# Performance work log

Measured on AMD Instinct MI355X. Metric: run time of the kernel, lower is better.

The kernel has to match this reference:

```python
import jax, jax.numpy as jnp
import numpy as np

EPS = 1e-5

def conv1x1(x, w, b):
    # x: [B,C,H,W], w: [O,C], b: [O]
    return jnp.einsum('bchw,oc->bohw', x, w) + b[None, :, None, None]

def bn(x, g, b, m, v):
    # eval-mode BatchNorm2d over channel axis 1
    s = g / jnp.sqrt(v + EPS)
    return (x - m[None, :, None, None]) * s[None, :, None, None] + b[None, :, None, None]

def setup_inputs() -> dict:
    key = jax.random.key(0)
    ks = jax.random.split(key, 12)
    B, C, Ci, H, W = 8, 512, 256, 64, 64
    d = {}
    d['x'] = jax.random.normal(ks[0], (B, C, H, W), jnp.float32)
    d['theta_w'] = jax.random.normal(ks[1], (Ci, C), jnp.float32) * (C ** -0.5)
    d['theta_b'] = jnp.zeros((Ci,), jnp.float32)
    d['theta_bn_g'] = jax.random.uniform(ks[2], (Ci,), jnp.float32, 0.5, 1.5)
    d['theta_bn_b'] = jax.random.normal(ks[3], (Ci,), jnp.float32) * 0.1
    d['theta_bn_m'] = jnp.zeros((Ci,), jnp.float32)
    d['theta_bn_v'] = jnp.ones((Ci,), jnp.float32)
    d['phi_w'] = jax.random.normal(ks[4], (Ci, C), jnp.float32) * (C ** -0.5)
    d['phi_b'] = jnp.zeros((Ci,), jnp.float32)
    d['phi_bn_g'] = jax.random.uniform(ks[5], (Ci,), jnp.float32, 0.5, 1.5)
    d['phi_bn_b'] = jax.random.normal(ks[6], (Ci,), jnp.float32) * 0.1
    d['phi_bn_m'] = jnp.zeros((Ci,), jnp.float32)
    d['phi_bn_v'] = jnp.ones((Ci,), jnp.float32)
    d['g_w'] = jax.random.normal(ks[7], (Ci, C), jnp.float32) * (C ** -0.5)
    d['g_b'] = jnp.zeros((Ci,), jnp.float32)
    d['wz_w'] = jax.random.normal(ks[8], (C, Ci), jnp.float32) * (Ci ** -0.5)
    d['wz_b'] = jnp.zeros((C,), jnp.float32)
    d['wz_bn_g'] = jax.random.uniform(ks[9], (C,), jnp.float32, 0.5, 1.5)
    d['wz_bn_b'] = jax.random.normal(ks[10], (C,), jnp.float32) * 0.1
    d['wz_bn_m'] = jnp.zeros((C,), jnp.float32)
    d['wz_bn_v'] = jnp.ones((C,), jnp.float32)
    return d

def reference(x, theta_w, theta_b, theta_bn_g, theta_bn_b, theta_bn_m, theta_bn_v,
              phi_w, phi_b, phi_bn_g, phi_bn_b, phi_bn_m, phi_bn_v,
              g_w, g_b, wz_w, wz_b, wz_bn_g, wz_bn_b, wz_bn_m, wz_bn_v):
    B, C, H, W = x.shape
    Ci = theta_w.shape[0]
    N = H * W
    scale = Ci ** -0.5
    th = bn(conv1x1(x, theta_w, theta_b), theta_bn_g, theta_bn_b, theta_bn_m, theta_bn_v).reshape(B, Ci, N)
    ph = bn(conv1x1(x, phi_w, phi_b), phi_bn_g, phi_bn_b, phi_bn_m, phi_bn_v).reshape(B, Ci, N)
    gx = conv1x1(x, g_w, g_b).reshape(B, Ci, N)
    # attn[b,n,m] = <theta[:,n], phi[:,m]> * scale, softmax over m (fp32 as in source)
    attn = jax.nn.softmax(jnp.einsum('bcn,bcm->bnm', th, ph) * scale, axis=-1)
    y = jnp.einsum('bnm,bcm->bcn', attn, gx).reshape(B, Ci, H, W)
    out = bn(conv1x1(y, wz_w, wz_b), wz_bn_g, wz_bn_b, wz_bn_m, wz_bn_v) + x
    return out
```

## Files before the change

kernel.cpp:

```cpp
#include <hip/hip_runtime.h>
#include <hip/hip_bf16.h>

typedef __attribute__((ext_vector_type(8))) short bf16x8;
typedef __attribute__((ext_vector_type(4))) float f32x4;
typedef __attribute__((ext_vector_type(16))) float f32x16;
typedef __attribute__((ext_vector_type(4))) unsigned short us4;
typedef __attribute__((ext_vector_type(8))) unsigned short us8;
typedef __attribute__((ext_vector_type(4))) unsigned int u32x4;

#define B_  8
#define C_  512
#define CI_ 256
#define N_  4096

__device__ __forceinline__ unsigned short f2b(float f) {
  unsigned u = __float_as_uint(f);
  u += 0x7FFFu + ((u >> 16) & 1u);
  return (unsigned short)(u >> 16);
}

__device__ __forceinline__ unsigned pkbf16(float lo, float hi) {
  union { __hip_bfloat162 h2; unsigned u; } cv;
  cv.h2 = __float22bfloat162_rn(make_float2(lo, hi));
  return cv.u;
}

__device__ __forceinline__ f32x4 mfma16(bf16x8 a, bf16x8 b, f32x4 c) {
  return __builtin_amdgcn_mfma_f32_16x16x32_bf16(a, b, c, 0, 0, 0);
}
__device__ __forceinline__ f32x16 mfma32(bf16x8 a, bf16x8 b, f32x16 c) {
  return __builtin_amdgcn_mfma_f32_32x32x16_bf16(a, b, c, 0, 0, 0);
}

__device__ __forceinline__ void gld16(const void* g, void* l) {
  __builtin_amdgcn_global_load_lds(
      (const __attribute__((address_space(1))) unsigned int*)g,
      (__attribute__((address_space(3))) unsigned int*)l, 16, 0, 0);
}

__global__ void fold_kernel(
  const float* __restrict__ thw, const float* __restrict__ thb,
  const float* __restrict__ thg, const float* __restrict__ thbb,
  const float* __restrict__ thm, const float* __restrict__ thv,
  const float* __restrict__ phw, const float* __restrict__ phb,
  const float* __restrict__ phg, const float* __restrict__ phbb,
  const float* __restrict__ phm, const float* __restrict__ phv,
  const float* __restrict__ gw,  const float* __restrict__ gb,
  const float* __restrict__ wzw, const float* __restrict__ wzb,
  const float* __restrict__ wzg, const float* __restrict__ wzbb,
  const float* __restrict__ wzm, const float* __restrict__ wzv,
  unsigned short* __restrict__ thW, unsigned short* __restrict__ phW,
  unsigned short* __restrict__ gW,  unsigned short* __restrict__ wzW,
  float* __restrict__ bTh, float* __restrict__ bPh,
  float* __restrict__ bG,  float* __restrict__ bWz)
{
  int i = blockIdx.x * 256 + threadIdx.x;
  const int WSZ = CI_ * C_;
  if (i < WSZ) { int o = i >> 9; thW[i] = f2b(thw[i] * (thg[o] * rsqrtf(thv[o] + 1e-5f))); return; }
  i -= WSZ;
  if (i < WSZ) { int o = i >> 9; phW[i] = f2b(phw[i] * (phg[o] * rsqrtf(phv[o] + 1e-5f))); return; }
  i -= WSZ;
  if (i < WSZ) { gW[i] = f2b(gw[i]); return; }
  i -= WSZ;
  if (i < WSZ) { int o = i >> 8; wzW[i] = f2b(wzw[i] * (wzg[o] * rsqrtf(wzv[o] + 1e-5f))); return; }
  i -= WSZ;
  if (i < CI_) { float s = thg[i] * rsqrtf(thv[i] + 1e-5f); bTh[i] = (thb[i] - thm[i]) * s + thbb[i]; return; }
  i -= CI_;
  if (i < CI_) { float s = phg[i] * rsqrtf(phv[i] + 1e-5f); bPh[i] = (phb[i] - phm[i]) * s + phbb[i]; return; }
  i -= CI_;
  if (i < CI_) { bG[i] = gb[i]; return; }
  i -= CI_;
  if (i < C_)  { float s = wzg[i] * rsqrtf(wzv[i] + 1e-5f); bWz[i] = (wzb[i] - wzm[i]) * s + wzbb[i]; return; }
}

__global__ __launch_bounds__(256) void transpose_cast(
  const float* __restrict__ x, unsigned short* __restrict__ xT)
{
  __shared__ float tl[64][68];
  const int b = blockIdx.z, c0 = blockIdx.y * 64, n0 = blockIdx.x * 64;
  const int t = threadIdx.x;
  const int r = t >> 2, q = (t & 3) * 16;
  const float* src = x + ((size_t)(b * C_ + c0 + r)) * N_ + n0 + q;
#pragma unroll
  for (int i = 0; i < 4; i++)
    *(f32x4*)&tl[r][q + i * 4] = *(const f32x4*)(src + i * 4);
  __syncthreads();
  unsigned short* dst = xT + ((size_t)(b * N_ + n0 + r)) * C_ + c0 + q;
  us8 o0, o1;
#pragma unroll
  for (int i = 0; i < 8; i++) o0[i] = f2b(tl[q + i][r]);
#pragma unroll
  for (int i = 0; i < 8; i++) o1[i] = f2b(tl[q + 8 + i][r]);
  *(us8*)dst = o0;
  *(us8*)(dst + 8) = o1;
}

template <int MODE>
__global__ __launch_bounds__(256, 2) void gemm_bt(
  const unsigned short* __restrict__ A,
  const unsigned short* __restrict__ Bm,
  const float* __restrict__ bias,
  const float* __restrict__ resid,
  void* __restrict__ outp,
  int Mdim, int Ndim, int Kdim)
{
  __shared__ __align__(16) unsigned short Al[2][128][64];
  __shared__ __align__(16) unsigned short Bl[2][128][64];
  const int b = blockIdx.z;
  const int m0 = blockIdx.y * 128;
  const int n0 = blockIdx.x * 128;
  const int t = threadIdx.x;
  const int w = t >> 6, l = t & 63, l15 = l & 15, g = l >> 4;
  const int wm = w >> 1, wn = w & 1;
  const int eg = l15 & 7;
  const unsigned short* Bb = Bm + (size_t)b * Ndim * Kdim;
  f32x4 acc[4][4];
#pragma unroll
  for (int i = 0; i < 4; i++)
#pragma unroll
    for (int j = 0; j < 4; j++) acc[i][j] = (f32x4){0.f, 0.f, 0.f, 0.f};

  int aoff[4], boff[4];
#pragma unroll
  for (int i = 0; i < 4; i++) {
    int j = w * 4 + i;
    int row = j * 8 + (l >> 3);
    int sw = ((l & 7) ^ (l >> 3)) * 8;
    aoff[i] = (m0 + row) * Kdim + sw;
    boff[i] = (n0 + row) * Kdim + sw;
  }

#define GSTAGE(bufv, k0v) do { \
    _Pragma("unroll") \
    for (int i_ = 0; i_ < 4; i_++) { \
      gld16(A  + aoff[i_] + (k0v), (unsigned char*)&Al[bufv][0][0] + (w * 4 + i_) * 1024); \
      gld16(Bb + boff[i_] + (k0v), (unsigned char*)&Bl[bufv][0][0] + (w * 4 + i_) * 1024); \
    } \
  } while (0)

  const int nk = Kdim >> 6;
  GSTAGE(0, 0);
  __syncthreads();
  for (int kk = 0; kk < nk; kk++) {
    if (kk + 1 < nk) GSTAGE((kk + 1) & 1, (kk + 1) * 64);
    const int cb = kk & 1;
#pragma unroll
    for (int ks = 0; ks < 2; ks++) {
      bf16x8 af[4], bfr[4];
#pragma unroll
      for (int i = 0; i < 4; i++)
        af[i]  = *(const bf16x8*)&Al[cb][wm * 64 + i * 16 + l15][((ks * 4 + g) ^ eg) * 8];
#pragma unroll
      for (int j = 0; j < 4; j++)
        bfr[j] = *(const bf16x8*)&Bl[cb][wn * 64 + j * 16 + l15][((ks * 4 + g) ^ eg) * 8];
#pragma unroll
      for (int i = 0; i < 4; i++)
#pragma unroll
        for (int j = 0; j < 4; j++)
          acc[i][j] = mfma16(af[i], bfr[j], acc[i][j]);
    }
    __syncthreads();
  }

#pragma unroll
  for (int i = 0; i < 4; i++) {
    int mrow = m0 + wm * 64 + i * 16 + 4 * g;
    f32x4 b4 = *(const f32x4*)&bias[mrow];
#pragma unroll
    for (int j = 0; j < 4; j++) {
      int n = n0 + wn * 64 + j * 16 + l15;
      f32x4 v = acc[i][j];
      v += b4;
      if constexpr (MODE == 0) {
        us4 pk = { f2b(v[0]), f2b(v[1]), f2b(v[2]), f2b(v[3]) };
        *(us4*)((unsigned short*)outp + ((size_t)b * Ndim + n) * Mdim + mrow) = pk;
      } else if constexpr (MODE == 1) {
        unsigned short* o = (unsigned short*)outp + ((size_t)b * Mdim + mrow) * (size_t)Ndim + n;
#pragma unroll
        for (int jj = 0; jj < 4; jj++) o[(size_t)jj * Ndim] = f2b(v[jj]);
      } else {
        size_t base = ((size_t)b * Mdim + mrow) * (size_t)Ndim + n;
        float* o = (float*)outp;
#pragma unroll
        for (int jj = 0; jj < 4; jj++)
          o[base + (size_t)jj * Ndim] = v[jj] + resid[base + (size_t)jj * Ndim];
      }
    }
  }
#undef GSTAGE
}

__global__ __launch_bounds__(512, 2) void attn_kernel(
  const unsigned short* __restrict__ thT,
  const unsigned short* __restrict__ phT,
  const unsigned short* __restrict__ gx,
  unsigned short* __restrict__ yT)
{
  __shared__ __align__(16) unsigned char lds[135168];
  const int t = threadIdx.x;
  const int w = t >> 6, l = t & 63, l31 = l & 31, h = l >> 5;
  const int qt = w & 3, mh = w >> 2;
  const int e7 = l31 & 7;
  const int id = blockIdx.x;
  const int b = id & 7;
  const int n0 = (id >> 3) * 128;
  const unsigned short* thB = thT + (size_t)b * N_ * CI_;
  const unsigned short* phB = phT + (size_t)b * N_ * CI_;
  const unsigned short* gxB = gx  + (size_t)b * CI_ * N_;

  const int kq = l >> 5, kc = l & 31;
  int koff[4];
#pragma unroll
  for (int i = 0; i < 4; i++) {
    int row = w * 8 + 2 * i + kq;
    koff[i] = row * 256 + ((kc ^ (row & 7)) * 8);
  }
  const int vq = l >> 3, vc = l & 7;
  int voff[4];
#pragma unroll
  for (int i = 0; i < 4; i++) {
    int ci = w * 32 + i * 8 + vq;
    voff[i] = ci * 4096 + ((vc ^ vq) * 8);
  }

#define STAGE(bufv, m0v) do { \
    const unsigned short* kg_ = phB + (size_t)(m0v) * 256; \
    const unsigned short* vg_ = gxB + (m0v); \
    unsigned base_ = (unsigned)(bufv) * 65536u + (unsigned)w * 4096u; \
    _Pragma("unroll") \
    for (int i_ = 0; i_ < 4; i_++) \
      gld16(kg_ + koff[i_], lds + base_ + i_ * 1024); \
    _Pragma("unroll") \
    for (int i_ = 0; i_ < 4; i_++) \
      gld16(vg_ + voff[i_], lds + base_ + 32768u + i_ * 1024); \
  } while (0)

  bf16x8 q[16];
  {
    const unsigned short* qp = thB + (size_t)(n0 + qt * 32 + l31) * CI_ + h * 8;
#pragma unroll
    for (int ks = 0; ks < 16; ks++) q[ks] = *(const bf16x8*)(qp + ks * 16);
  }

  f32x16 acc[8];
#pragma unroll
  for (int i = 0; i < 8; i++)
#pragma unroll
    for (int r = 0; r < 16; r++) acc[i][r] = 0.f;
  float M = -1e30f, L = 0.f;
  const float kS = 0.0625f * 1.44269504f;

  STAGE(0, 0);
  __syncthreads();
  int cur = 0;

  for (int tt = 0; tt < 64; tt++) {
    const int m0 = tt * 64;
    if (tt < 63) STAGE(cur ^ 1, m0 + 64);
    const unsigned char* kb = lds + cur * 65536;
    const unsigned char* vb = kb + 32768;

    f32x16 S;
#pragma unroll
    for (int r = 0; r < 16; r++) S[r] = 0.f;
#pragma unroll
    for (int ks = 0; ks < 16; ks++) {
      bf16x8 kf = *(const bf16x8*)(kb + (mh * 32 + l31) * 512 + ((((ks * 2 + h)) ^ e7) << 4));
      S = mfma32(kf, q[ks], S);
    }

    float pm = S[0];
#pragma unroll
    for (int r = 1; r < 16; r++) pm = fmaxf(pm, S[r]);
    pm *= kS;
    pm = fmaxf(pm, __shfl_xor(pm, 32));
    int dfr = __all(pm <= M + 8.0f);
    if (!dfr) {
      float nm = fmaxf(M, pm);
      float rs = exp2f(M - nm);
      M = nm; L *= rs;
#pragma unroll
      for (int r = 0; r < 16; r++) {
        float rr = __shfl(rs, h * 32 + ((r & 3) + 8 * (r >> 2) + 4 * h));
#pragma unroll
        for (int c = 0; c < 8; c++) acc[c][r] *= rr;
      }
    }
    float p[16];
    float rsum = 0.f;
#pragma unroll
    for (int r = 0; r < 16; r++) {
      p[r] = exp2f(S[r] * kS - M);
      rsum += p[r];
    }
    rsum += __shfl_xor(rsum, 32);
    L += rsum;

    unsigned pk[8];
#pragma unroll
    for (int qq = 0; qq < 8; qq++)
      pk[qq] = pkbf16(p[2 * qq], p[2 * qq + 1]);

#pragma unroll
    for (int ks = 0; ks < 2; ks++) {
      unsigned s00 = pk[ks * 4 + 0], s10 = pk[ks * 4 + 2];
      unsigned s01 = pk[ks * 4 + 1], s11 = pk[ks * 4 + 3];
      unsigned own0 = h ? s10 : s00;
      unsigned snd0 = h ? s00 : s10;
      unsigned own1 = h ? s11 : s01;
      unsigned snd1 = h ? s01 : s11;
      unsigned sw0 = (unsigned)__shfl_xor((int)snd0, 32);
      unsigned sw1 = (unsigned)__shfl_xor((int)snd1, 32);
      u32x4 pv;
      pv[0] = h ? sw0 : own0;
      pv[1] = h ? sw1 : own1;
      pv[2] = h ? own0 : sw0;
      pv[3] = h ? own1 : sw1;
      bf16x8 pa = *(bf16x8*)&pv;
      const int gidx = mh * 4 + ks * 2 + h;
#pragma unroll
      for (int cit = 0; cit < 8; cit++) {
        bf16x8 vf = *(const bf16x8*)(vb + (cit * 32 + l31) * 128 + ((gidx ^ e7) << 4));
        acc[cit] = mfma32(pa, vf, acc[cit]);
      }
    }
    __syncthreads();
    cur ^= 1;
  }

  float* MB = (float*)(lds + 131072);
  float* LB = (float*)(lds + 131072 + 2048);
  MB[mh * 256 + qt * 64 + l] = M;
  LB[mh * 256 + qt * 64 + l] = L;
  float* ab = (float*)lds + qt * 8192 + l;
  if (mh) {
#pragma unroll
    for (int cit = 0; cit < 8; cit++)
#pragma unroll
      for (int r = 0; r < 16; r++)
        ab[(cit * 16 + r) * 64] = acc[cit][r];
  }
  __syncthreads();
  if (!mh) {
    unsigned short* yB = yT + (size_t)b * N_ * CI_;
#pragma unroll
    for (int r = 0; r < 16; r++) {
      int nl = (r & 3) + 8 * (r >> 2) + 4 * h;
      int li = qt * 64 + h * 32 + nl;
      float M1 = MB[li], L1 = LB[li];
      float M2 = MB[256 + li], L2 = LB[256 + li];
      float Mf = fmaxf(M1, M2);
      float s1 = exp2f(M1 - Mf), s2 = exp2f(M2 - Mf);
      float invf = 1.0f / (L1 * s1 + L2 * s2);
      s1 *= invf; s2 *= invf;
      int n = n0 + qt * 32 + nl;
#pragma unroll
      for (int cit = 0; cit < 8; cit++) {
        float v = acc[cit][r] * s1 + ab[(cit * 16 + r) * 64] * s2;
        yB[(size_t)n * CI_ + cit * 32 + l31] = f2b(v);
      }
    }
  }
#undef STAGE
}

extern "C" void kernel_launch(void* const* d_in, const int* in_sizes, int n_in,
                              void* d_out, int out_size, void* d_ws, size_t ws_size,
                              hipStream_t stream)
{
  const float* x    = (const float*)d_in[0];
  const float* thw  = (const float*)d_in[1];
  const float* thb  = (const float*)d_in[2];
  const float* thg  = (const float*)d_in[3];
  const float* thbb = (const float*)d_in[4];
  const float* thm  = (const float*)d_in[5];
  const float* thv  = (const float*)d_in[6];
  const float* phw  = (const float*)d_in[7];
  const float* phb  = (const float*)d_in[8];
  const float* phg  = (const float*)d_in[9];
  const float* phbb = (const float*)d_in[10];
  const float* phm  = (const float*)d_in[11];
  const float* phv  = (const float*)d_in[12];
  const float* gw   = (const float*)d_in[13];
  const float* gb   = (const float*)d_in[14];
  const float* wzw  = (const float*)d_in[15];
  const float* wzb  = (const float*)d_in[16];
  const float* wzg  = (const float*)d_in[17];
  const float* wzbb = (const float*)d_in[18];
  const float* wzm  = (const float*)d_in[19];
  const float* wzv  = (const float*)d_in[20];

  char* ws = (char*)d_ws;
  unsigned short* xbT = (unsigned short*)(ws);
  unsigned short* thT = (unsigned short*)(ws + 33554432ull);
  unsigned short* phT = (unsigned short*)(ws + 50331648ull);
  unsigned short* gxb = (unsigned short*)(ws + 67108864ull);
  unsigned short* yT  = (unsigned short*)(ws + 83886080ull);
  unsigned short* thW = (unsigned short*)(ws + 100663296ull);
  unsigned short* phW = (unsigned short*)(ws + 100925440ull);
  unsigned short* gW  = (unsigned short*)(ws + 101187584ull);
  unsigned short* wzW = (unsigned short*)(ws + 101449728ull);
  float* bTh = (float*)(ws + 101711872ull);
  float* bPh = (float*)(ws + 101712896ull);
  float* bG  = (float*)(ws + 101713920ull);
  float* bWz = (float*)(ws + 101714944ull);

  fold_kernel<<<2053, 256, 0, stream>>>(
      thw, thb, thg, thbb, thm, thv,
      phw, phb, phg, phbb, phm, phv,
      gw, gb, wzw, wzb, wzg, wzbb, wzm, wzv,
      thW, phW, gW, wzW, bTh, bPh, bG, bWz);

  transpose_cast<<<dim3(64, 8, 8), 256, 0, stream>>>(x, xbT);

  gemm_bt<0><<<dim3(32, 2, 8), 256, 0, stream>>>(thW, xbT, bTh, nullptr, thT, CI_, N_, C_);
  gemm_bt<0><<<dim3(32, 2, 8), 256, 0, stream>>>(phW, xbT, bPh, nullptr, phT, CI_, N_, C_);
  gemm_bt<1><<<dim3(32, 2, 8), 256, 0, stream>>>(gW,  xbT, bG,  nullptr, gxb, CI_, N_, C_);

  attn_kernel<<<dim3(256), 512, 0, stream>>>(thT, phT, gxb, yT);

  gemm_bt<2><<<dim3(32, 4, 8), 256, 0, stream>>>(wzW, yT, bWz, x, d_out, C_, N_, CI_);
}
```

Before: 279.7 us.

## Shrink attention blocks to 256 threads with single-buffered LDS and bf16 merge

The attention kernel now runs 512 blocks of 4 waves, each covering 64 queries, instead of 256 blocks of 8 waves covering 128. The K/V tiles are single-buffered and staged at the top of each iteration behind a barrier, which halves LDS use so more blocks can be resident per CU. Each wave now issues twice as many global-to-LDS loads per stage. The cross-half partial accumulators are packed to bf16 for the final merge to save LDS space. The cost is that load latency is no longer overlapped within a block, only across co-resident blocks, and the merge loses some precision.

```diff
diff --git a/kernel.cpp b/kernel.cpp
--- a/kernel.cpp
+++ b/kernel.cpp
@@ -190,49 +190,48 @@
 #undef GSTAGE
 }
 
-__global__ __launch_bounds__(512, 2) void attn_kernel(
+__global__ __launch_bounds__(256, 2) void attn_kernel(
   const unsigned short* __restrict__ thT,
   const unsigned short* __restrict__ phT,
   const unsigned short* __restrict__ gx,
   unsigned short* __restrict__ yT)
 {
-  __shared__ __align__(16) unsigned char lds[135168];
+  __shared__ __align__(16) unsigned char lds[67584];
   const int t = threadIdx.x;
   const int w = t >> 6, l = t & 63, l31 = l & 31, h = l >> 5;
-  const int qt = w & 3, mh = w >> 2;
+  const int qt = w & 1, mh = w >> 1;
   const int e7 = l31 & 7;
   const int id = blockIdx.x;
   const int b = id & 7;
-  const int n0 = (id >> 3) * 128;
+  const int n0 = (id >> 3) * 64;
   const unsigned short* thB = thT + (size_t)b * N_ * CI_;
   const unsigned short* phB = phT + (size_t)b * N_ * CI_;
   const unsigned short* gxB = gx  + (size_t)b * CI_ * N_;
 
   const int kq = l >> 5, kc = l & 31;
-  int koff[4];
-#pragma unroll
-  for (int i = 0; i < 4; i++) {
-    int row = w * 8 + 2 * i + kq;
+  int koff[8];
+#pragma unroll
+  for (int i = 0; i < 8; i++) {
+    int row = w * 16 + 2 * i + kq;
     koff[i] = row * 256 + ((kc ^ (row & 7)) * 8);
   }
   const int vq = l >> 3, vc = l & 7;
-  int voff[4];
-#pragma unroll
-  for (int i = 0; i < 4; i++) {
-    int ci = w * 32 + i * 8 + vq;
+  int voff[8];
+#pragma unroll
+  for (int i = 0; i < 8; i++) {
+    int ci = w * 64 + i * 8 + vq;
     voff[i] = ci * 4096 + ((vc ^ vq) * 8);
   }
 
-#define STAGE(bufv, m0v) do { \
+#define STAGE(m0v) do { \
     const unsigned short* kg_ = phB + (size_t)(m0v) * 256; \
     const unsigned short* vg_ = gxB + (m0v); \
-    unsigned base_ = (unsigned)(bufv) * 65536u + (unsigned)w * 4096u; \
     _Pragma("unroll") \
-    for (int i_ = 0; i_ < 4; i_++) \
-      gld16(kg_ + koff[i_], lds + base_ + i_ * 1024); \
+    for (int i_ = 0; i_ < 8; i_++) \
+      gld16(kg_ + koff[i_], lds + (unsigned)w * 8192u + i_ * 1024u); \
     _Pragma("unroll") \
-    for (int i_ = 0; i_ < 4; i_++) \
-      gld16(vg_ + voff[i_], lds + base_ + 32768u + i_ * 1024); \
+    for (int i_ = 0; i_ < 8; i_++) \
+      gld16(vg_ + voff[i_], lds + 32768u + (unsigned)w * 8192u + i_ * 1024u); \
   } while (0)
 
   bf16x8 q[16];
@@ -250,15 +249,11 @@
   float M = -1e30f, L = 0.f;
   const float kS = 0.0625f * 1.44269504f;
 
-  STAGE(0, 0);
-  __syncthreads();
-  int cur = 0;
-
   for (int tt = 0; tt < 64; tt++) {
-    const int m0 = tt * 64;
-    if (tt < 63) STAGE(cur ^ 1, m0 + 64);
-    const unsigned char* kb = lds + cur * 65536;
-    const unsigned char* vb = kb + 32768;
+    STAGE(tt * 64);
+    __syncthreads();
+    const unsigned char* kb = lds;
+    const unsigned char* vb = lds + 32768;
 
     f32x16 S;
 #pragma unroll
@@ -325,20 +320,19 @@
       }
     }
     __syncthreads();
-    cur ^= 1;
-  }
-
-  float* MB = (float*)(lds + 131072);
-  float* LB = (float*)(lds + 131072 + 2048);
-  MB[mh * 256 + qt * 64 + l] = M;
-  LB[mh * 256 + qt * 64 + l] = L;
-  float* ab = (float*)lds + qt * 8192 + l;
+  }
+
+  float* MB = (float*)(lds + 65536);
+  float* LB = (float*)(lds + 66560);
+  MB[mh * 128 + qt * 64 + l] = M;
+  LB[mh * 128 + qt * 64 + l] = L;
+  unsigned* ab32 = (unsigned*)(lds + qt * 16384);
   if (mh) {
 #pragma unroll
     for (int cit = 0; cit < 8; cit++)
 #pragma unroll
-      for (int r = 0; r < 16; r++)
-        ab[(cit * 16 + r) * 64] = acc[cit][r];
+      for (int pr = 0; pr < 8; pr++)
+        ab32[(cit * 8 + pr) * 64 + l] = pkbf16(acc[cit][2 * pr], acc[cit][2 * pr + 1]);
   }
   __syncthreads();
   if (!mh) {
@@ -348,15 +342,19 @@
       int nl = (r & 3) + 8 * (r >> 2) + 4 * h;
       int li = qt * 64 + h * 32 + nl;
       float M1 = MB[li], L1 = LB[li];
-      float M2 = MB[256 + li], L2 = LB[256 + li];
+      float M2 = MB[128 + li], L2 = LB[128 + li];
       float Mf = fmaxf(M1, M2);
       float s1 = exp2f(M1 - Mf), s2 = exp2f(M2 - Mf);
       float invf = 1.0f / (L1 * s1 + L2 * s2);
       s1 *= invf; s2 *= invf;
       int n = n0 + qt * 32 + nl;
+      const int pr = r >> 1;
 #pragma unroll
       for (int cit = 0; cit < 8; cit++) {
-        float v = acc[cit][r] * s1 + ab[(cit * 16 + r) * 64] * s2;
+        unsigned v2 = ab32[(cit * 8 + pr) * 64 + l];
+        unsigned bits = (r & 1) ? (v2 & 0xFFFF0000u) : (v2 << 16);
+        float other = __uint_as_float(bits);
+        float v = acc[cit][r] * s1 + other * s2;
         yB[(size_t)n * CI_ + cit * 32 + l31] = f2b(v);
       }
     }
@@ -417,7 +415,7 @@
   gemm_bt<0><<<dim3(32, 2, 8), 256, 0, stream>>>(phW, xbT, bPh, nullptr, phT, CI_, N_, C_);
   gemm_bt<1><<<dim3(32, 2, 8), 256, 0, stream>>>(gW,  xbT, bG,  nullptr, gxb, CI_, N_, C_);
 
-  attn_kernel<<<dim3(256), 512, 0, stream>>>(thT, phT, gxb, yT);
+  attn_kernel<<<dim3(512), 256, 0, stream>>>(thT, phT, gxb, yT);
 
   gemm_bt<2><<<dim3(32, 4, 8), 256, 0, stream>>>(wzW, yT, bWz, x, d_out, C_, N_, CI_);
 }
```

Result: slower. 286.5 us (+2.4%).
